# Kernel tuning notes

Hardware: AMD Instinct MI355X
Metric: run time of the kernel (lower is better)

## Reference

```python
import jax, jax.numpy as jnp
import numpy as np

# Scattering2D hyperparameters (kymatio-style Morlet filter bank)
J, L, M, N = 2, 8, 224, 224
SIGMA0 = 0.8
XI0 = 3.0 * np.pi / 4.0
SLANT = 4.0 / L


def _fold(h, k):
    """Fourier-domain subsampling / filter periodization: fold and average k x k blocks."""
    if k == 1:
        return h
    Mh, Nh = h.shape[-2], h.shape[-1]
    return h.reshape(h.shape[:-2] + (k, Mh // k, k, Nh // k)).mean(axis=(-4, -2))


def _freq_grid():
    wx = (2 * np.pi * np.fft.fftfreq(M)).astype(np.float64)[:, None]
    wy = (2 * np.pi * np.fft.fftfreq(N)).astype(np.float64)[None, :]
    return wx, wy


def _morlet_hat(theta, xi, sigma):
    wx, wy = _freq_grid()
    u = np.cos(theta) * wx + np.sin(theta) * wy
    v = -np.sin(theta) * wx + np.cos(theta) * wy
    gab = np.exp(-0.5 * sigma ** 2 * ((u - xi) ** 2 + (v / SLANT) ** 2))
    gauss = np.exp(-0.5 * sigma ** 2 * (u ** 2 + (v / SLANT) ** 2))
    kappa = np.exp(-0.5 * sigma ** 2 * xi ** 2)  # zero-mean Morlet correction
    return (gab - kappa * gauss).astype(np.float32)


def _build_filters():
    psi = {}
    for j in range(J):
        f = np.stack([_morlet_hat(l * np.pi / L, XI0 / 2 ** j, SIGMA0 * 2 ** j) for l in range(L)])
        psi[j] = [_fold(f, 2 ** r) for r in range(j + 1)]  # periodized to each resolution
    wx, wy = _freq_grid()
    sig_phi = SIGMA0 * 2 ** (J - 1)
    phi0 = np.exp(-0.5 * sig_phi ** 2 * (wx ** 2 + wy ** 2)).astype(np.float32)
    phi = [_fold(phi0, 2 ** r) for r in range(J)]
    return psi, phi


PSI, PHI = _build_filters()


def _scattering(x):
    # x: (B, C, M, N) float32 -> (B, C, K, M/2^J, N/2^J), K = 1 + J*L + L^2*J*(J-1)/2
    xh = jnp.fft.fft2(x)
    s0 = jnp.fft.ifft2(_fold(xh * PHI[0], 2 ** J)).real[..., None, :, :]
    s1s, s2s = [], []
    for j1 in range(J):
        # first order: bandpass, subsample to resolution j1, modulus
        u1h = _fold(xh[..., None, :, :] * PSI[j1][0], 2 ** j1)       # (B,C,L,M/2^j1,N/2^j1)
        u1 = jnp.abs(jnp.fft.ifft2(u1h))
        u1h2 = jnp.fft.fft2(u1)
        s1s.append(jnp.fft.ifft2(_fold(u1h2 * PHI[j1], 2 ** (J - j1))).real)
        for j2 in range(j1 + 1, J):
            # second order over all (theta1, theta2) pairs, vectorized over L x L
            u2h = _fold(u1h2[..., None, :, :] * PSI[j2][j1], 2 ** (j2 - j1))  # (B,C,L,L,.,.)
            u2 = jnp.abs(jnp.fft.ifft2(u2h))
            s2 = jnp.fft.ifft2(_fold(jnp.fft.fft2(u2) * PHI[j2], 2 ** (J - j2))).real
            s2s.append(s2.reshape(s2.shape[:2] + (L * L,) + s2.shape[-2:]))
    return jnp.concatenate([s0] + s1s + s2s, axis=2)


def setup_inputs() -> dict:
    key = jax.random.key(0)
    k1, k2, _ = jax.random.split(key, 3)
    x = jax.random.normal(k1, (16, 3, M, N), dtype=jnp.float32)
    W_last = jax.random.normal(k2, (1000, 243), dtype=jnp.float32) * 0.02
    b_last = jnp.zeros((1000,), dtype=jnp.float32)
    return {"x": x, "W_last": W_last, "b_last": b_last}


def reference(x, W_last, b_last):
    s = _scattering(x)                                   # (B, 3, 81, 56, 56)
    B = s.shape[0]
    s = s.reshape(B, s.shape[1] * s.shape[2], s.shape[3], s.shape[4])  # flatten(1,2)
    g = s.max(axis=(-2, -1))                             # global max pool -> (B, 243)
    return g @ W_last.T + b_last                         # (B, 1000)
```

## Files before the change

### kernel.cpp

```cpp
#include <hip/hip_runtime.h>
#include <math.h>

#define PI_D 3.14159265358979323846

#define IMG224 50176
#define IMG112 12544
static const size_t OFF_FT224F = 0;
static const size_t OFF_FT224I = 2048;
static const size_t OFF_FT112F = 4096;
static const size_t OFF_FT112I = 6144;
static const size_t OFF_FT56I  = 8192;
static const size_t OFF_PHW    = 8600;
static const size_t OFF_PSI   = 257152;
static const size_t OFF_PHI0  = 1059968;
static const size_t OFF_PHI1  = 1110144;
static const size_t OFF_GK    = 1122688;
static const size_t OFF_XH    = 1126784;
static const size_t OFF_POOL  = 5943680;

__device__ inline unsigned fkey(float v) {
    int b = __float_as_int(v);
    return (b >= 0) ? ((unsigned)b | 0x80000000u) : ~(unsigned)b;
}
__device__ inline float funkey(unsigned u) {
    int b = (u & 0x80000000u) ? (int)(u & 0x7fffffffu) : (int)~u;
    return __int_as_float(b);
}
__device__ inline void cmac(float2& a, float2 z, float2 w) {
    a.x += z.x * w.x - z.y * w.y;
    a.y += z.x * w.y + z.y * w.x;
}
__device__ inline float2 cmulc(float2 v, float c, float s) {
    return make_float2(v.x * c - v.y * s, v.x * s + v.y * c);
}

template<int SGN>
__device__ inline void fft16(float2* x) {
    const float C8  = 0.70710678118654752f;
    const float C16 = 0.92387953251128674f;
    const float S16 = 0.38268343236508977f;
    const float sg = (float)SGN;
    float2 g[16];
#pragma unroll
    for (int b = 0; b < 4; ++b) {
        float2 x0 = x[b], x1 = x[4 + b], x2 = x[8 + b], x3 = x[12 + b];
        float2 e0 = make_float2(x0.x + x2.x, x0.y + x2.y);
        float2 e1 = make_float2(x0.x - x2.x, x0.y - x2.y);
        float2 o0 = make_float2(x1.x + x3.x, x1.y + x3.y);
// ... 15 lines not shown
    g[14] = cmulc(g[14], -C8,  sg * C8);
    g[15] = cmulc(g[15], -C16, -sg * S16);
#pragma unroll
    for (int p = 0; p < 4; ++p) {
        float2 x0 = g[p], x1 = g[4 + p], x2 = g[8 + p], x3 = g[12 + p];
        float2 e0 = make_float2(x0.x + x2.x, x0.y + x2.y);
        float2 e1 = make_float2(x0.x - x2.x, x0.y - x2.y);
        float2 o0 = make_float2(x1.x + x3.x, x1.y + x3.y);
        float2 o1 = make_float2(x1.x - x3.x, x1.y - x3.y);
        float2 io1 = (SGN > 0) ? make_float2(-o1.y, o1.x) : make_float2(o1.y, -o1.x);
        x[p + 0]  = make_float2(e0.x + o0.x, e0.y + o0.y);
        x[p + 8]  = make_float2(e0.x - o0.x, e0.y - o0.y);
        x[p + 4]  = make_float2(e1.x + io1.x, e1.y + io1.y);
        x[p + 12] = make_float2(e1.x - io1.x, e1.y - io1.y);
    }
}

template<int SGN>
__device__ inline void fft8(float2* x) {
    const float C8 = 0.70710678118654752f;
    const float sg = (float)SGN;
    float2 E[4], O[4];
    {
        float2 e0 = make_float2(x[0].x + x[4].x, x[0].y + x[4].y);
        float2 e1 = make_float2(x[0].x - x[4].x, x[0].y - x[4].y);
        float2 o0 = make_float2(x[2].x + x[6].x, x[2].y + x[6].y);
        float2 o1 = make_float2(x[2].x - x[6].x, x[2].y - x[6].y);
        float2 io1 = (SGN > 0) ? make_float2(-o1.y, o1.x) : make_float2(o1.y, -o1.x);
        E[0] = make_float2(e0.x + o0.x, e0.y + o0.y);
        E[2] = make_float2(e0.x - o0.x, e0.y - o0.y);
        E[1] = make_float2(e1.x + io1.x, e1.y + io1.y);
        E[3] = make_float2(e1.x - io1.x, e1.y - io1.y);
    }
    {
        float2 e0 = make_float2(x[1].x + x[5].x, x[1].y + x[5].y);
        float2 e1 = make_float2(x[1].x - x[5].x, x[1].y - x[5].y);
        float2 o0 = make_float2(x[3].x + x[7].x, x[3].y + x[7].y);
        float2 o1 = make_float2(x[3].x - x[7].x, x[3].y - x[7].y);
        float2 io1 = (SGN > 0) ? make_float2(-o1.y, o1.x) : make_float2(o1.y, -o1.x);
        O[0] = make_float2(e0.x + o0.x, e0.y + o0.y);
        O[2] = make_float2(e0.x - o0.x, e0.y - o0.y);
        O[1] = make_float2(e1.x + io1.x, e1.y + io1.y);
        O[3] = make_float2(e1.x - io1.x, e1.y - io1.y);
    }
    float2 t0 = O[0];
    float2 t1 = cmulc(O[1], C8, sg * C8);
    float2 t2 = (SGN > 0) ? make_float2(-O[2].y, O[2].x) : make_float2(O[2].y, -O[2].x);
    float2 t3 = cmulc(O[3], -C8, sg * C8);
    x[0] = make_float2(E[0].x + t0.x, E[0].y + t0.y);
    x[4] = make_float2(E[0].x - t0.x, E[0].y - t0.y);
    x[1] = make_float2(E[1].x + t1.x, E[1].y + t1.y);
    x[5] = make_float2(E[1].x - t1.x, E[1].y - t1.y);
    x[2] = make_float2(E[2].x + t2.x, E[2].y + t2.y);
    x[6] = make_float2(E[2].x - t2.x, E[2].y - t2.y);
    x[3] = make_float2(E[3].x + t3.x, E[3].y + t3.y);
    x[7] = make_float2(E[3].x - t3.x, E[3].y - t3.y);
}

__global__ void k_fact(float2* o, int N1, int N2, double sign, double scale, int r2) {
    int base3 = N1 * N1 + N2 * N2 + N2 * N1;
    int total = base3 + (r2 ? 63 : 0);
    int N = N1 * N2;
    for (int i = blockIdx.x * blockDim.x + threadIdx.x; i < total; i += blockDim.x * gridDim.x) {
        double ang; double sc = 1.0;
        if (i < N1 * N1) {
            int n1 = i / N1, k1 = i % N1;
            ang = sign * 2.0 * PI_D * (double)((n1 * k1) % N1) / (double)N1;
        } else if (i < N1 * N1 + N2 * N2) {
            int j = i - N1 * N1; int n2 = j / N2, k2 = j % N2;
            ang = sign * 2.0 * PI_D * (double)((n2 * k2) % N2) / (double)N2;
            sc = scale;
// ... 24 lines not shown
    double wy = 2.0 * PI_D * fc / 224.0;
    double theta = (double)l * PI_D / 8.0;
    double xi = (3.0 * PI_D / 4.0) / (double)(1 << j);
    double sg = 0.8 * (double)(1 << j);
    double ct = cos(theta), st = sin(theta);
    double u = ct * wx + st * wy;
    double v = -st * wx + ct * wy;
    double vs = v / 0.5;
    double s2 = 0.5 * sg * sg;
    double gab = exp(-s2 * ((u - xi) * (u - xi) + vs * vs));
    double gau = exp(-s2 * (u * u + vs * vs));
    double kap = exp(-s2 * xi * xi);
    out[i] = (float)(gab - kap * gau);
}

__global__ void k_phi(float* phi0, float* phi1, float* taps) {
    int i = blockIdx.x * blockDim.x + threadIdx.x;
    const double sp = 1.6;
    const double s2 = 0.5 * sp * sp;
    if (i < IMG224) {
        int r = i / 224, c = i % 224;
        double fr = (r < 112) ? (double)r : (double)(r - 224);
        double fc = (c < 112) ? (double)c : (double)(c - 224);
        double wx = 2.0 * PI_D * fr / 224.0;
        double wy = 2.0 * PI_D * fc / 224.0;
        phi0[i] = (float)exp(-s2 * (wx * wx + wy * wy));
    } else if (i < IMG224 + IMG112) {
        int p = i - IMG224, a = p / 112, b = p % 112;
        double sum = 0.0;
        for (int ii = 0; ii < 2; ++ii)
            for (int jj = 0; jj < 2; ++jj) {
                int r = a + 112 * ii, c = b + 112 * jj;
                double fr = (r < 112) ? (double)r : (double)(r - 224);
                double fc = (c < 112) ? (double)c : (double)(c - 224);
                double wx = 2.0 * PI_D * fr / 224.0;
                double wy = 2.0 * PI_D * fc / 224.0;
                sum += exp(-s2 * (wx * wx + wy * wy));
            }
        phi1[p] = (float)(0.25 * sum);
    } else if (i < IMG224 + IMG112 + 16) {
        int m = i - (IMG224 + IMG112);
        double acc = 0.0;
        for (int k = 0; k < 112; ++k) {
            double fr0 = (double)k;
            double fr1 = (double)(k - 112);
            double w0 = 2.0 * PI_D * fr0 / 224.0;
            double w1 = 2.0 * PI_D * fr1 / 224.0;
            double F112 = 0.5 * (exp(-s2 * w0 * w0) + exp(-s2 * w1 * w1));
            acc += F112 * cos(2.0 * PI_D * (double)k * (double)m / 112.0);
        }
        taps[m] = (float)(acc / 112.0);
    }
}

__global__ void k_zero(unsigned* gk, int n) {
    int i = blockIdx.x * blockDim.x + threadIdx.x;
    if (i < n) gk[i] = 0u;
}

template<int N1, int N2, int TA, int FOLD, int BS, bool REAL, int SGN>
__global__ __launch_bounds__(BS) void rk(
    const void* __restrict__ inBase, int inShift,
    const float* __restrict__ fltBase, int fltMask,
    const float2* __restrict__ FT, float2* __restrict__ out,
    int swzImg, int inStride, int inOff)
{
// ... 46 lines not shown
                        float f = flt[idx];
                        re += v.x * f; im += v.y * f;
                    }
                Z[r * ZS + b] = make_float2(re * s, im * s);
            }
        }
    }
    __syncthreads();
    for (int idx = t; idx < TA * N2 * 2; idx += BS) {
        int r = idx / (N2 * 2);
        int rem = idx % (N2 * 2);
        int n2 = rem / 2, h = rem % 2;
        float2 xx[N1];
#pragma unroll
        for (int n1 = 0; n1 < N1; ++n1) xx[n1] = Z[r * ZS + n1 * N2 + n2];
        if constexpr (N1 == 16) fft16<SGN>(xx); else fft8<SGN>(xx);
#pragma unroll
        for (int kk = 0; kk < K1H; ++kk) {
            int k1 = h * K1H + kk;
            float2 tw = TW[n2 * N1 + k1];
            T[r * TS + n2 * (N1 + 1) + k1] = cmulc(xx[k1], tw.x, tw.y);
        }
    }
    __syncthreads();
    if constexpr (N2 == 14) {
        const float2* W7  = FT + N1 * N1 + N2 * N2 + N2 * N1;
        const float2* T14 = W7 + 49;
        for (int idx = t; idx < TA * N1; idx += BS) {
            int r = idx / N1, k1 = idx % N1;
            float2 E[7], O[7];
#pragma unroll
            for (int k = 0; k < 7; ++k) { E[k] = make_float2(0.f, 0.f); O[k] = make_float2(0.f, 0.f); }
            for (int m = 0; m < 7; ++m) {
                float2 te = T[r * TS + (2 * m) * (N1 + 1) + k1];
                float2 to = T[r * TS + (2 * m + 1) * (N1 + 1) + k1];
#pragma unroll
                for (int k = 0; k < 7; ++k) {
                    float2 w = W7[m * 7 + k];
                    cmac(E[k], te, w);
                    cmac(O[k], to, w);
                }
            }
#pragma unroll
            for (int k = 0; k < 14; ++k) {
                float2 tw = T14[k];
                float2 o_ = O[k % 7];
                float2 X = E[k % 7];
                X.x += o_.x * tw.x - o_.y * tw.y;
                X.y += o_.x * tw.y + o_.y * tw.x;
                Z[r * ZS + k1 + N1 * k] = X;
            }
        }
    } else {
        for (int idx = t; idx < TA * N1; idx += BS) {
            int r = idx / N1, k1 = idx % N1;
            float2 acc[N2];
#pragma unroll
            for (int kk = 0; kk < N2; ++kk) acc[kk] = make_float2(0.f, 0.f);
            for (int n2 = 0; n2 < N2; ++n2) {
                float2 tv = T[r * TS + n2 * (N1 + 1) + k1];
#pragma unroll
                for (int kk = 0; kk < N2; ++kk) cmac(acc[kk], tv, W2[n2 * N2 + kk]);
            }
#pragma unroll
            for (int kk = 0; kk < N2; ++kk) Z[r * ZS + k1 + N1 * kk] = acc[kk];
        }
    }
    __syncthreads();
#pragma unroll
    for (int r = 0; r < TA; ++r) {
        float2* o = out + ((size_t)gOut * N + (a0 + r)) * N;
        for (int b = t; b < N; b += BS) o[b] = Z[r * ZS + b];
    }
}

template<int N1, int N2, int SPLIT, int BS, int SGN>
__global__ __launch_bounds__(BS) void ck1(
    const float2* __restrict__ in, const float2* __restrict__ FT, float2* __restrict__ out)
{
    constexpr int N = N1 * N2;
// ... 18 lines not shown
        float2 tw = TW[n2 * N1 + k1];
        float2 r0 = cmulc(a0[k1], tw.x, tw.y);
        float2 r1 = cmulc(a1[k1], tw.x, tw.y);
        *reinterpret_cast<float4*>(&out[((size_t)g * N + (k1 * N2 + n2)) * N + b0]) =
            make_float4(r0.x, r0.y, r1.x, r1.y);
    }
}

template<int N1, int N2, int SPLIT, int MODE, int BS>
__global__ __launch_bounds__(BS) void ck2(
    const float2* __restrict__ in, const float2* __restrict__ FT,
    float2* __restrict__ outc, float* __restrict__ outr)
{
    constexpr int N = N1 * N2;
    constexpr int NC = N / SPLIT;
    const float2* W2 = FT + N1 * N1;
    const int g = blockIdx.x / SPLIT, half = blockIdx.x % SPLIT;
    const int k1 = blockIdx.y, t = threadIdx.x;
    if (2 * t >= NC) return;
    const int b0 = 2 * t + half * NC;
    const float2* I = in + (size_t)g * N * N;
    if constexpr (N2 == 14) {
        const float2* W7  = FT + N1 * N1 + N2 * N2 + N2 * N1;
        const float2* T14 = W7 + 49;
        float2 E0[7], E1[7], O0[7], O1[7];
#pragma unroll
        for (int k = 0; k < 7; ++k) {
            E0[k] = make_float2(0.f, 0.f); E1[k] = make_float2(0.f, 0.f);
            O0[k] = make_float2(0.f, 0.f); O1[k] = make_float2(0.f, 0.f);
        }
#pragma unroll
        for (int m = 0; m < 7; ++m) {
            float4 ve = *reinterpret_cast<const float4*>(&I[(size_t)(k1 * 14 + 2 * m) * N + b0]);
            float4 vo = *reinterpret_cast<const float4*>(&I[(size_t)(k1 * 14 + 2 * m + 1) * N + b0]);
            float2 ve0 = make_float2(ve.x, ve.y), ve1 = make_float2(ve.z, ve.w);
            float2 vo0 = make_float2(vo.x, vo.y), vo1 = make_float2(vo.z, vo.w);
#pragma unroll
            for (int k = 0; k < 7; ++k) {
                float2 w = W7[m * 7 + k];
                cmac(E0[k], ve0, w); cmac(E1[k], ve1, w);
                cmac(O0[k], vo0, w); cmac(O1[k], vo1, w);
            }
        }
#pragma unroll
        for (int k = 0; k < 14; ++k) {
            float2 tw = T14[k];
            float2 r0 = E0[k % 7], r1 = E1[k % 7];
            float2 o0 = O0[k % 7], o1 = O1[k % 7];
            r0.x += o0.x * tw.x - o0.y * tw.y;
            r0.y += o0.x * tw.y + o0.y * tw.x;
            r1.x += o1.x * tw.x - o1.y * tw.y;
            r1.y += o1.x * tw.y + o1.y * tw.x;
            if (MODE == 0) {
                *reinterpret_cast<float4*>(&outc[((size_t)g * N + (k1 + N1 * k)) * N + b0]) =
                    make_float4(r0.x, r0.y, r1.x, r1.y);
            } else {
                size_t o = ((size_t)g * N + (k1 + N1 * k)) * N + b0;
                outr[o]     = sqrtf(r0.x * r0.x + r0.y * r0.y);
                outr[o + 1] = sqrtf(r1.x * r1.x + r1.y * r1.y);
            }
        }
    } else {
        float2 acc[N2][2];
#pragma unroll
        for (int k2 = 0; k2 < N2; ++k2) { acc[k2][0] = make_float2(0.f, 0.f); acc[k2][1] = make_float2(0.f, 0.f); }
#pragma unroll
        for (int n2 = 0; n2 < N2; ++n2) {
            float4 v = *reinterpret_cast<const float4*>(&I[(size_t)(k1 * N2 + n2) * N + b0]);
            float2 v0 = make_float2(v.x, v.y), v1 = make_float2(v.z, v.w);
#pragma unroll
            for (int k2 = 0; k2 < N2; ++k2) {
                float2 w = W2[n2 * N2 + k2];
                cmac(acc[k2][0], v0, w);
                cmac(acc[k2][1], v1, w);
            }
        }
        if (MODE == 0) {
#pragma unroll
            for (int k2 = 0; k2 < N2; ++k2)
                *reinterpret_cast<float4*>(&outc[((size_t)g * N + (k1 + N1 * k2)) * N + b0]) =
                    make_float4(acc[k2][0].x, acc[k2][0].y, acc[k2][1].x, acc[k2][1].y);
        } else {
#pragma unroll
            for (int k2 = 0; k2 < N2; ++k2) {
                size_t o = ((size_t)g * N + (k1 + N1 * k2)) * N + b0;
                outr[o]     = sqrtf(acc[k2][0].x * acc[k2][0].x + acc[k2][0].y * acc[k2][0].y);
                outr[o + 1] = sqrtf(acc[k2][1].x * acc[k2][1].x + acc[k2][1].y * acc[k2][1].y);
            }
        }
    }
}

template<int SGN, int BS, int EPI>
__device__ inline void fft112_2d(float2* Z, const float2* __restrict__ FT, int t)
{
    constexpr int ZS = 113;
    constexpr int NCH = (112 * 16 + BS - 1) / BS;
    const float2* W2 = FT + 256;
    const float2* TW = FT + 256 + 49;
    const float s7 = W2[0].x;
    float wr[3][3], wi[3][3];
#pragma unroll
    for (int m = 1; m <= 3; ++m)
#pragma unroll
        for (int k = 1; k <= 3; ++k) {
            float2 w = W2[m * 7 + k];
            wr[m - 1][k - 1] = w.x;
            wi[m - 1][k - 1] = w.y;
        }
    for (int idx = t; idx < 112 * 7; idx += BS) {
        int r = idx % 112, n2 = idx / 112;
        float2 xx[16];
#pragma unroll
        for (int n1 = 0; n1 < 16; ++n1) xx[n1] = Z[r * ZS + n1 * 7 + n2];
        fft16<SGN>(xx);
#pragma unroll
        for (int k1 = 0; k1 < 16; ++k1) {
            float2 tw = TW[n2 * 16 + k1];
            Z[r * ZS + k1 * 7 + n2] = cmulc(xx[k1], tw.x, tw.y);
        }
    }
    __syncthreads();
    {
        float2 tv[NCH][7];
#pragma unroll
        for (int c = 0; c < NCH; ++c) {
            int idx = c * BS + t;
            if (idx < 112 * 16) {
                int r = idx >> 4, k1 = idx & 15;
#pragma unroll
                for (int m = 0; m < 7; ++m) tv[c][m] = Z[r * ZS + k1 * 7 + m];
            }
        }
        __syncthreads();
#pragma unroll
        for (int c = 0; c < NCH; ++c) {
            int idx = c * BS + t;
            if (idx < 112 * 16) {
                int r = idx >> 4, k1 = idx & 15;
                float2 t0 = tv[c][0];
                float2 a1 = make_float2(tv[c][1].x + tv[c][6].x, tv[c][1].y + tv[c][6].y);
                float2 b1 = make_float2(tv[c][1].x - tv[c][6].x, tv[c][1].y - tv[c][6].y);
                float2 a2 = make_float2(tv[c][2].x + tv[c][5].x, tv[c][2].y + tv[c][5].y);
                float2 b2 = make_float2(tv[c][2].x - tv[c][5].x, tv[c][2].y - tv[c][5].y);
                float2 a3 = make_float2(tv[c][3].x + tv[c][4].x, tv[c][3].y + tv[c][4].y);
                float2 b3 = make_float2(tv[c][3].x - tv[c][4].x, tv[c][3].y - tv[c][4].y);
                float bx = s7 * t0.x, by = s7 * t0.y;
                Z[r * ZS + k1] = make_float2(s7 * (t0.x + a1.x + a2.x + a3.x),
                                             s7 * (t0.y + a1.y + a2.y + a3.y));
#pragma unroll
                for (int k = 0; k < 3; ++k) {
                    float Px = wr[0][k] * a1.x + wr[1][k] * a2.x + wr[2][k] * a3.x;
                    float Py = wr[0][k] * a1.y + wr[1][k] * a2.y + wr[2][k] * a3.y;
                    float Qx = wi[0][k] * b1.x + wi[1][k] * b2.x + wi[2][k] * b3.x;
                    float Qy = wi[0][k] * b1.y + wi[1][k] * b2.y + wi[2][k] * b3.y;
                    Z[r * ZS + k1 + 16 * (k + 1)] = make_float2(bx + Px - Qy, by + Py + Qx);
                    Z[r * ZS + k1 + 16 * (6 - k)] = make_float2(bx + Px + Qy, by + Py - Qx);
                }
            }
        }
    }
    __syncthreads();
    for (int idx = t; idx < 112 * 7; idx += BS) {
        int b = idx % 112, n2 = idx / 112;
        float2 xx[16];
#pragma unroll
        for (int n1 = 0; n1 < 16; ++n1) xx[n1] = Z[(n1 * 7 + n2) * ZS + b];
        fft16<SGN>(xx);
#pragma unroll
        for (int k1 = 0; k1 < 16; ++k1) {
            float2 tw = TW[n2 * 16 + k1];
            Z[(k1 * 7 + n2) * ZS + b] = cmulc(xx[k1], tw.x, tw.y);
        }
// ... 4 lines not shown
#pragma unroll
        for (int c = 0; c < NCH; ++c) {
            int idx = c * BS + t;
            if (idx < 112 * 16) {
                int b = idx >> 4, k1 = idx & 15;
#pragma unroll
                for (int m = 0; m < 7; ++m) tv[c][m] = Z[(k1 * 7 + m) * ZS + b];
            }
        }
        __syncthreads();
#pragma unroll
        for (int c = 0; c < NCH; ++c) {
            int idx = c * BS + t;
            if (idx < 112 * 16) {
                int b = idx >> 4, k1 = idx & 15;
                float2 t0 = tv[c][0];
                float2 a1 = make_float2(tv[c][1].x + tv[c][6].x, tv[c][1].y + tv[c][6].y);
                float2 b1 = make_float2(tv[c][1].x - tv[c][6].x, tv[c][1].y - tv[c][6].y);
                float2 a2 = make_float2(tv[c][2].x + tv[c][5].x, tv[c][2].y + tv[c][5].y);
                float2 b2 = make_float2(tv[c][2].x - tv[c][5].x, tv[c][2].y - tv[c][5].y);
                float2 a3 = make_float2(tv[c][3].x + tv[c][4].x, tv[c][3].y + tv[c][4].y);
                float2 b3 = make_float2(tv[c][3].x - tv[c][4].x, tv[c][3].y - tv[c][4].y);
                float bxr = s7 * t0.x, byr = s7 * t0.y;
                {
                    float X = s7 * (t0.x + a1.x + a2.x + a3.x);
                    float Y = s7 * (t0.y + a1.y + a2.y + a3.y);
                    Z[k1 * ZS + b] = EPI ? make_float2(sqrtf(X * X + Y * Y), 0.f)
                                         : make_float2(X, Y);
                }
#pragma unroll
                for (int k = 0; k < 3; ++k) {
                    float Px = wr[0][k] * a1.x + wr[1][k] * a2.x + wr[2][k] * a3.x;
                    float Py = wr[0][k] * a1.y + wr[1][k] * a2.y + wr[2][k] * a3.y;
                    float Qx = wi[0][k] * b1.x + wi[1][k] * b2.x + wi[2][k] * b3.x;
                    float Qy = wi[0][k] * b1.y + wi[1][k] * b2.y + wi[2][k] * b3.y;
                    float X1 = bxr + Px - Qy, Y1 = byr + Py + Qx;
                    float X2 = bxr + Px + Qy, Y2 = byr + Py - Qx;
                    Z[(k1 + 16 * (k + 1)) * ZS + b] =
                        EPI ? make_float2(sqrtf(X1 * X1 + Y1 * Y1), 0.f) : make_float2(X1, Y1);
                    Z[(k1 + 16 * (6 - k)) * ZS + b] =
                        EPI ? make_float2(sqrtf(X2 * X2 + Y2 * Y2), 0.f) : make_float2(X2, Y2);
                }
            }
        }
    }
    __syncthreads();
}

template<int BS>
__global__ __launch_bounds__(BS) void sc2pipe(
    const float2* __restrict__ inBase, const float* __restrict__ psiBase,
    const float* __restrict__ taps, const float2* __restrict__ FTI,
    unsigned* __restrict__ gk, int slotBase, int inStride, int subShift)
{
    constexpr int ZS = 113;
    __shared__ float2 Z[112 * ZS];
// ... 53 lines not shown
            int rb = r0 + m; rb -= (rb >= 112) ? 112 : 0;
            acc += gw[m] * (Ft[ra * 57 + j] + Ft[rb * 57 + j]);
        }
        mx = fmaxf(mx, acc);
    }
    for (int off = 32; off > 0; off >>= 1) mx = fmaxf(mx, __shfl_down(mx, off, 64));
    if ((t & 63) == 0) red[t >> 6] = mx;
    __syncthreads();
    if (t == 0) {
#pragma unroll
        for (int w = 1; w < BS / 64; ++w) mx = fmaxf(mx, red[w]);
        atomicMax(&gk[img * 81 + slotBase + sub], fkey(mx));
    }
}

template<int FOLD, int BS>
__global__ __launch_bounds__(BS) void s56max(
    const float2* __restrict__ in, const float* __restrict__ flt,
    const float2* __restrict__ FT, unsigned* __restrict__ gk,
    int slotBase, int slotShift, int slotMask)
{
    constexpr int N = 56, NIN = 56 * FOLD, ZS = 57;
    __shared__ float2 Z[N * ZS];
    __shared__ float2 T[N * ZS];
    __shared__ float red[BS / 64];
    const float2* W2 = FT + 64;
    const float2* TW = FT + 64 + 49;
    const int g = blockIdx.x, t = threadIdx.x;
    const float2* I = in + (size_t)g * NIN * NIN;
    const float s = 1.0f / (float)(FOLD * FOLD);
#pragma unroll 4
    for (int idx = t; idx < N * N; idx += BS) {
        int r = idx / N, b = idx % N;
        float re = 0.f, im = 0.f;
#pragma unroll
        for (int i = 0; i < FOLD; ++i)
#pragma unroll
            for (int j = 0; j < FOLD; ++j) {
                int p = (r + N * i) * NIN + (b + N * j);
                float2 v = I[p];
                float f = flt[p];
                re += v.x * f; im += v.y * f;
            }
        Z[r * ZS + b] = make_float2(re * s, im * s);
    }
    __syncthreads();
    for (int idx = t; idx < 7 * N; idx += BS) {
        int n2 = idx / N, r = idx % N;
        float2 xx[8];
#pragma unroll
        for (int n1 = 0; n1 < 8; ++n1) xx[n1] = Z[r * ZS + n1 * 7 + n2];
        fft8<1>(xx);
#pragma unroll
        for (int k1 = 0; k1 < 8; ++k1) {
            float2 tw = TW[n2 * 8 + k1];
            T[r * ZS + k1 * 7 + n2] = cmulc(xx[k1], tw.x, tw.y);
        }
    }
    __syncthreads();
    for (int idx = t; idx < 8 * N; idx += BS) {
        int k1 = idx / N, r = idx % N;
        float2 tv[7];
#pragma unroll
        for (int n2 = 0; n2 < 7; ++n2) tv[n2] = T[r * ZS + k1 * 7 + n2];
#pragma unroll
        for (int k2 = 0; k2 < 7; ++k2) {
            float2 acc = make_float2(0.f, 0.f);
#pragma unroll
            for (int n2 = 0; n2 < 7; ++n2) cmac(acc, tv[n2], W2[n2 * 7 + k2]);
            Z[r * ZS + k1 + 8 * k2] = acc;
        }
    }
    __syncthreads();
    for (int idx = t; idx < 7 * N; idx += BS) {
        int n2 = idx / N, b = idx % N;
        float2 xx[8];
#pragma unroll
        for (int n1 = 0; n1 < 8; ++n1) xx[n1] = Z[(n1 * 7 + n2) * ZS + b];
        fft8<1>(xx);
#pragma unroll
        for (int k1 = 0; k1 < 8; ++k1) {
            float2 tw = TW[n2 * 8 + k1];
            T[(k1 * 7 + n2) * ZS + b] = cmulc(xx[k1], tw.x, tw.y);
        }
    }
    __syncthreads();
    float m = -INFINITY;
    for (int idx = t; idx < 8 * N; idx += BS) {
        int k1 = idx / N, b = idx % N;
        float2 tv[7];
#pragma unroll
        for (int n2 = 0; n2 < 7; ++n2) tv[n2] = T[(k1 * 7 + n2) * ZS + b];
#pragma unroll
        for (int k2 = 0; k2 < 7; ++k2) {
            float re = 0.f;
#pragma unroll
            for (int n2 = 0; n2 < 7; ++n2) {
                float2 w = W2[n2 * 7 + k2];
                re += tv[n2].x * w.x - tv[n2].y * w.y;
            }
            m = fmaxf(m, re);
        }
    }
    for (int off = 32; off > 0; off >>= 1) m = fmaxf(m, __shfl_down(m, off, 64));
    if ((t & 63) == 0) red[t >> 6] = m;
    __syncthreads();
    if (t == 0) {
#pragma unroll
        for (int w = 1; w < BS / 64; ++w) m = fmaxf(m, red[w]);
        int slot = slotBase + ((g >> slotShift) * 81) + (g & slotMask);
        atomicMax(&gk[slot], fkey(m));
    }
}

__global__ void k_linear(const unsigned* __restrict__ gk, const float* __restrict__ Wl,
                         const float* __restrict__ bl, float* __restrict__ out)
{
    int i = blockIdx.x * blockDim.x + threadIdx.x;
    if (i >= 16 * 1000) return;
    int b = i / 1000, o = i % 1000;
    float s = bl[o];
    for (int f = 0; f < 243; ++f)
        s += funkey(gk[b * 243 + f]) * Wl[o * 243 + f];
    out[i] = s;
}

extern "C" void kernel_launch(void* const* d_in, const int* in_sizes, int n_in,
                              void* d_out, int out_size, void* d_ws, size_t ws_size,
                              hipStream_t stream)
{
    const float* x  = (const float*)d_in[0];
    const float* Wl = (const float*)d_in[1];
    const float* bl = (const float*)d_in[2];
    float* out = (float*)d_out;
    float* ws = (float*)d_ws;

    float2* FT224F = (float2*)(ws + OFF_FT224F);
    float2* FT224I = (float2*)(ws + OFF_FT224I);
    float2* FT112F = (float2*)(ws + OFF_FT112F);
    float2* FT112I = (float2*)(ws + OFF_FT112I);
    float2* FT56I  = (float2*)(ws + OFF_FT56I);
    float* TAPS = ws + OFF_PHW;
    float* PSI0 = ws + OFF_PSI;
    float* PSI1 = ws + OFF_PSI + 8 * IMG224;
    float* PHI0 = ws + OFF_PHI0;
    float* PHI1 = ws + OFF_PHI1;
    unsigned* GK = (unsigned*)(ws + OFF_GK);
    float2* XH  = (float2*)(ws + OFF_XH);
    float* A0  = ws + OFF_POOL;
    float* A1  = A0 + 9633792;
    float* A23 = A1 + 9633792;

    k_fact<<<4, 256, 0, stream>>>(FT224F, 16, 14, -1.0, 1.0, 1);
    k_fact<<<4, 256, 0, stream>>>(FT224I, 16, 14,  1.0, 1.0 / 224.0, 1);
    k_fact<<<4, 256, 0, stream>>>(FT112F, 16, 7,  -1.0, 1.0, 0);
    k_fact<<<4, 256, 0, stream>>>(FT112I, 16, 7,   1.0, 1.0 / 112.0, 0);
    k_fact<<<1, 256, 0, stream>>>(FT56I,  8, 7,    1.0, 1.0 / 56.0, 0);
    k_psi<<<(16 * IMG224 + 255) / 256, 256, 0, stream>>>(ws + OFF_PSI);
    k_phi<<<(IMG224 + IMG112 + 16 + 255) / 256, 256, 0, stream>>>(PHI0, PHI1, TAPS);
    k_zero<<<(3888 + 255) / 256, 256, 0, stream>>>(GK, 3888);

    rk<16, 14, 4, 1, 128, true, -1><<<dim3(48, 56), 128, 0, stream>>>(x, 0, nullptr, 0, FT224F, (float2*)A0, 0, 0, 0);
    ck1<16, 14, 2, 64, -1><<<dim3(96, 14), 64, 0, stream>>>((float2*)A0, FT224F, (float2*)A1);
    ck2<16, 14, 2, 0, 64><<<dim3(96, 16), 64, 0, stream>>>((float2*)A1, FT224F, XH, nullptr);

    s56max<4, 256><<<48, 256, 0, stream>>>(XH, PHI0, FT56I, GK, 0, 0, 0);

    sc2pipe<1024><<<384, 1024, 0, stream>>>(XH, PSI1, TAPS, FT112I, GK, 9, 1, 3);

    for (int c = 0; c < 4; ++c) {
        rk<16, 14, 4, 1, 128, false, 1><<<dim3(96, 56), 128, 0, stream>>>(
            XH, 1, PSI0 + (size_t)(2 * c) * IMG224, 1, FT224I, (float2*)A0, -1, 0, 0);
        ck1<16, 14, 2, 64, 1><<<dim3(192, 14), 64, 0, stream>>>((float2*)A0, FT224I, (float2*)A1);
        ck2<16, 14, 2, 1, 64><<<dim3(192, 16), 64, 0, stream>>>((float2*)A1, FT224I, nullptr, A23);
        rk<16, 14, 4, 1, 128, true, -1><<<dim3(96, 56), 128, 0, stream>>>(A23, 0, nullptr, 0, FT224F, (float2*)A0, 0, 0, 0);
        ck1<16, 14, 2, 64, -1><<<dim3(192, 14), 64, 0, stream>>>((float2*)A0, FT224F, (float2*)A1);
        ck2<16, 14, 2, 0, 64><<<dim3(192, 16), 64, 0, stream>>>((float2*)A1, FT224F, (float2*)A0, nullptr);
        s56max<4, 256><<<96, 256, 0, stream>>>((float2*)A0, PHI0, FT56I, GK, 1 + 2 * c, 1, 1);
        sc2pipe<1024><<<768, 1024, 0, stream>>>((float2*)A0, PSI1, TAPS, FT112I, GK, 17 + 16 * c, 2, 4);
    }

    k_linear<<<(16000 + 255) / 256, 256, 0, stream>>>(GK, Wl, bl, out);
}
```

Measured before the change: 1.068 ms.

## Replace Fourier-domain lowpass/fold/iFFT with spatial separable conv and use symmetric DFT7

The order-0 and order-1 lowpass outputs are now computed directly in the spatial domain as a separable 23-tap circular convolution, evaluated only at every fourth row and column, with precomputed taps. This replaces the Fourier multiply, fold and 56x56 inverse FFT (s56max). The order-1 pass runs on the real modulus image before its forward FFT. The column-pass DFT7 in ck2 now uses the shared symmetric-pair dft7 helper instead of a dense 7x7 complex matmul. The unused phi filters and 112/56 twiddle tables are dropped. The spatial conv truncates the Gaussian kernel to 11 taps per side, which introduces a small approximation.

```diff
diff --git a/kernel.cpp b/kernel.cpp
--- a/kernel.cpp
+++ b/kernel.cpp
@@ -9,11 +9,8 @@
 static const size_t OFF_FT224I = 2048;
 static const size_t OFF_FT112F = 4096;
 static const size_t OFF_FT112I = 6144;
-static const size_t OFF_FT56I  = 8192;
 static const size_t OFF_PHW    = 8600;
 static const size_t OFF_PSI   = 257152;
-static const size_t OFF_PHI0  = 1059968;
-static const size_t OFF_PHI1  = 1110144;
 static const size_t OFF_GK    = 1122688;
 static const size_t OFF_XH    = 1126784;
 static const size_t OFF_POOL  = 5943680;
@@ -32,6 +29,39 @@
 }
 __device__ inline float2 cmulc(float2 v, float c, float s) {
     return make_float2(v.x * c - v.y * s, v.x * s + v.y * c);
+}
+
+struct C7 { float s; float wr[3][3]; float wi[3][3]; };
+__device__ inline void ld7(const float2* __restrict__ W7, C7& c) {
+    c.s = W7[0].x;
+#pragma unroll
+    for (int m = 1; m <= 3; ++m)
+#pragma unroll
+        for (int k = 1; k <= 3; ++k) {
+            float2 w = W7[m * 7 + k];
+            c.wr[m - 1][k - 1] = w.x;
+            c.wi[m - 1][k - 1] = w.y;
+        }
+}
+__device__ inline void dft7(const C7& c, const float2 t[7], float2 X[7]) {
+    float2 a1 = make_float2(t[1].x + t[6].x, t[1].y + t[6].y);
+    float2 b1 = make_float2(t[1].x - t[6].x, t[1].y - t[6].y);
+    float2 a2 = make_float2(t[2].x + t[5].x, t[2].y + t[5].y);
+    float2 b2 = make_float2(t[2].x - t[5].x, t[2].y - t[5].y);
+    float2 a3 = make_float2(t[3].x + t[4].x, t[3].y + t[4].y);
+    float2 b3 = make_float2(t[3].x - t[4].x, t[3].y - t[4].y);
+    float bx = c.s * t[0].x, by = c.s * t[0].y;
+    X[0] = make_float2(c.s * (t[0].x + a1.x + a2.x + a3.x),
+                       c.s * (t[0].y + a1.y + a2.y + a3.y));
+#pragma unroll
+    for (int k = 0; k < 3; ++k) {
+        float Px = c.wr[0][k] * a1.x + c.wr[1][k] * a2.x + c.wr[2][k] * a3.x;
+        float Py = c.wr[0][k] * a1.y + c.wr[1][k] * a2.y + c.wr[2][k] * a3.y;
+        float Qx = c.wi[0][k] * b1.x + c.wi[1][k] * b2.x + c.wi[2][k] * b3.x;
+        float Qy = c.wi[0][k] * b1.y + c.wi[1][k] * b2.y + c.wi[2][k] * b3.y;
+        X[k + 1] = make_float2(bx + Px - Qy, by + Py + Qx);
+        X[6 - k] = make_float2(bx + Px + Qy, by + Py - Qx);
+    }
 }
 
 template<int SGN>
@@ -77,47 +107,6 @@
         x[p + 4]  = make_float2(e1.x + io1.x, e1.y + io1.y);
         x[p + 12] = make_float2(e1.x - io1.x, e1.y - io1.y);
     }
-}
-
-template<int SGN>
-__device__ inline void fft8(float2* x) {
-    const float C8 = 0.70710678118654752f;
-    const float sg = (float)SGN;
-    float2 E[4], O[4];
-    {
-        float2 e0 = make_float2(x[0].x + x[4].x, x[0].y + x[4].y);
-        float2 e1 = make_float2(x[0].x - x[4].x, x[0].y - x[4].y);
-        float2 o0 = make_float2(x[2].x + x[6].x, x[2].y + x[6].y);
-        float2 o1 = make_float2(x[2].x - x[6].x, x[2].y - x[6].y);
-        float2 io1 = (SGN > 0) ? make_float2(-o1.y, o1.x) : make_float2(o1.y, -o1.x);
-        E[0] = make_float2(e0.x + o0.x, e0.y + o0.y);
-        E[2] = make_float2(e0.x - o0.x, e0.y - o0.y);
-        E[1] = make_float2(e1.x + io1.x, e1.y + io1.y);
-        E[3] = make_float2(e1.x - io1.x, e1.y - io1.y);
-    }
-    {
-        float2 e0 = make_float2(x[1].x + x[5].x, x[1].y + x[5].y);
-        float2 e1 = make_float2(x[1].x - x[5].x, x[1].y - x[5].y);
-        float2 o0 = make_float2(x[3].x + x[7].x, x[3].y + x[7].y);
-        float2 o1 = make_float2(x[3].x - x[7].x, x[3].y - x[7].y);
-        float2 io1 = (SGN > 0) ? make_float2(-o1.y, o1.x) : make_float2(o1.y, -o1.x);
-        O[0] = make_float2(e0.x + o0.x, e0.y + o0.y);
-        O[2] = make_float2(e0.x - o0.x, e0.y - o0.y);
-        O[1] = make_float2(e1.x + io1.x, e1.y + io1.y);
-        O[3] = make_float2(e1.x - io1.x, e1.y - io1.y);
-    }
-    float2 t0 = O[0];
-    float2 t1 = cmulc(O[1], C8, sg * C8);
-    float2 t2 = (SGN > 0) ? make_float2(-O[2].y, O[2].x) : make_float2(O[2].y, -O[2].x);
-    float2 t3 = cmulc(O[3], -C8, sg * C8);
-    x[0] = make_float2(E[0].x + t0.x, E[0].y + t0.y);
-    x[4] = make_float2(E[0].x - t0.x, E[0].y - t0.y);
-    x[1] = make_float2(E[1].x + t1.x, E[1].y + t1.y);
-    x[5] = make_float2(E[1].x - t1.x, E[1].y - t1.y);
-    x[2] = make_float2(E[2].x + t2.x, E[2].y + t2.y);
-    x[6] = make_float2(E[2].x - t2.x, E[2].y - t2.y);
-    x[3] = make_float2(E[3].x + t3.x, E[3].y + t3.y);
-    x[7] = make_float2(E[3].x - t3.x, E[3].y - t3.y);
 }
 
 __global__ void k_fact(float2* o, int N1, int N2, double sign, double scale, int r2) {
@@ -172,42 +161,27 @@
     out[i] = (float)(gab - kap * gau);
 }
 
-__global__ void k_phi(float* phi0, float* phi1, float* taps) {
+__global__ void k_taps(float* taps) {
     int i = blockIdx.x * blockDim.x + threadIdx.x;
-    const double sp = 1.6;
-    const double s2 = 0.5 * sp * sp;
-    if (i < IMG224) {
-        int r = i / 224, c = i % 224;
-        double fr = (r < 112) ? (double)r : (double)(r - 224);
-        double fc = (c < 112) ? (double)c : (double)(c - 224);
-        double wx = 2.0 * PI_D * fr / 224.0;
-        double wy = 2.0 * PI_D * fc / 224.0;
-        phi0[i] = (float)exp(-s2 * (wx * wx + wy * wy));
-    } else if (i < IMG224 + IMG112) {
-        int p = i - IMG224, a = p / 112, b = p % 112;
-        double sum = 0.0;
-        for (int ii = 0; ii < 2; ++ii)
-            for (int jj = 0; jj < 2; ++jj) {
-                int r = a + 112 * ii, c = b + 112 * jj;
-                double fr = (r < 112) ? (double)r : (double)(r - 224);
-                double fc = (c < 112) ? (double)c : (double)(c - 224);
-                double wx = 2.0 * PI_D * fr / 224.0;
-                double wy = 2.0 * PI_D * fc / 224.0;
-                sum += exp(-s2 * (wx * wx + wy * wy));
-            }
-        phi1[p] = (float)(0.25 * sum);
-    } else if (i < IMG224 + IMG112 + 16) {
-        int m = i - (IMG224 + IMG112);
+    const double s2 = 0.5 * 1.6 * 1.6;
+    if (i < 16) {
         double acc = 0.0;
         for (int k = 0; k < 112; ++k) {
-            double fr0 = (double)k;
-            double fr1 = (double)(k - 112);
-            double w0 = 2.0 * PI_D * fr0 / 224.0;
-            double w1 = 2.0 * PI_D * fr1 / 224.0;
-            double F112 = 0.5 * (exp(-s2 * w0 * w0) + exp(-s2 * w1 * w1));
-            acc += F112 * cos(2.0 * PI_D * (double)k * (double)m / 112.0);
-        }
-        taps[m] = (float)(acc / 112.0);
+            double w0 = 2.0 * PI_D * (double)k / 224.0;
+            double w1 = 2.0 * PI_D * (double)(k - 112) / 224.0;
+            double F = 0.5 * (exp(-s2 * w0 * w0) + exp(-s2 * w1 * w1));
+            acc += F * cos(2.0 * PI_D * (double)k * (double)i / 112.0);
+        }
+        taps[i] = (float)(acc / 112.0);
+    } else if (i < 32) {
+        int m = i - 16;
+        double acc = 0.0;
+        for (int k = 0; k < 224; ++k) {
+            double fr = (k < 112) ? (double)k : (double)(k - 224);
+            double w = 2.0 * PI_D * fr / 224.0;
+            acc += exp(-s2 * w * w) * cos(2.0 * PI_D * (double)k * (double)m / 224.0);
+        }
+        taps[i] = (float)(acc / 224.0);
     }
 }
 
@@ -284,7 +258,7 @@
         float2 xx[N1];
 #pragma unroll
         for (int n1 = 0; n1 < N1; ++n1) xx[n1] = Z[r * ZS + n1 * N2 + n2];
-        if constexpr (N1 == 16) fft16<SGN>(xx); else fft8<SGN>(xx);
+        fft16<SGN>(xx);
 #pragma unroll
         for (int kk = 0; kk < K1H; ++kk) {
             int k1 = h * K1H + kk;
@@ -293,7 +267,7 @@
         }
     }
     __syncthreads();
-    if constexpr (N2 == 14) {
+    {
         const float2* W7  = FT + N1 * N1 + N2 * N2 + N2 * N1;
         const float2* T14 = W7 + 49;
         for (int idx = t; idx < TA * N1; idx += BS) {
@@ -320,20 +294,6 @@
                 X.y += o_.x * tw.y + o_.y * tw.x;
                 Z[r * ZS + k1 + N1 * k] = X;
             }
-        }
-    } else {
-        for (int idx = t; idx < TA * N1; idx += BS) {
-            int r = idx / N1, k1 = idx % N1;
-            float2 acc[N2];
-#pragma unroll
-            for (int kk = 0; kk < N2; ++kk) acc[kk] = make_float2(0.f, 0.f);
-            for (int n2 = 0; n2 < N2; ++n2) {
-                float2 tv = T[r * TS + n2 * (N1 + 1) + k1];
-#pragma unroll
-                for (int kk = 0; kk < N2; ++kk) cmac(acc[kk], tv, W2[n2 * N2 + kk]);
-            }
-#pragma unroll
-            for (int kk = 0; kk < N2; ++kk) Z[r * ZS + k1 + N1 * kk] = acc[kk];
         }
     }
     __syncthreads();
@@ -382,79 +342,48 @@
 {
     constexpr int N = N1 * N2;
     constexpr int NC = N / SPLIT;
-    const float2* W2 = FT + N1 * N1;
     const int g = blockIdx.x / SPLIT, half = blockIdx.x % SPLIT;
     const int k1 = blockIdx.y, t = threadIdx.x;
     if (2 * t >= NC) return;
     const int b0 = 2 * t + half * NC;
     const float2* I = in + (size_t)g * N * N;
-    if constexpr (N2 == 14) {
-        const float2* W7  = FT + N1 * N1 + N2 * N2 + N2 * N1;
-        const float2* T14 = W7 + 49;
-        float2 E0[7], E1[7], O0[7], O1[7];
-#pragma unroll
-        for (int k = 0; k < 7; ++k) {
-            E0[k] = make_float2(0.f, 0.f); E1[k] = make_float2(0.f, 0.f);
-            O0[k] = make_float2(0.f, 0.f); O1[k] = make_float2(0.f, 0.f);
-        }
-#pragma unroll
-        for (int m = 0; m < 7; ++m) {
-            float4 ve = *reinterpret_cast<const float4*>(&I[(size_t)(k1 * 14 + 2 * m) * N + b0]);
-            float4 vo = *reinterpret_cast<const float4*>(&I[(size_t)(k1 * 14 + 2 * m + 1) * N + b0]);
-            float2 ve0 = make_float2(ve.x, ve.y), ve1 = make_float2(ve.z, ve.w);
-            float2 vo0 = make_float2(vo.x, vo.y), vo1 = make_float2(vo.z, vo.w);
-#pragma unroll
-            for (int k = 0; k < 7; ++k) {
-                float2 w = W7[m * 7 + k];
-                cmac(E0[k], ve0, w); cmac(E1[k], ve1, w);
-                cmac(O0[k], vo0, w); cmac(O1[k], vo1, w);
-            }
-        }
-#pragma unroll
-        for (int k = 0; k < 14; ++k) {
-            float2 tw = T14[k];
-            float2 r0 = E0[k % 7], r1 = E1[k % 7];
-            float2 o0 = O0[k % 7], o1 = O1[k % 7];
-            r0.x += o0.x * tw.x - o0.y * tw.y;
-            r0.y += o0.x * tw.y + o0.y * tw.x;
-            r1.x += o1.x * tw.x - o1.y * tw.y;
-            r1.y += o1.x * tw.y + o1.y * tw.x;
-            if (MODE == 0) {
-                *reinterpret_cast<float4*>(&outc[((size_t)g * N + (k1 + N1 * k)) * N + b0]) =
-                    make_float4(r0.x, r0.y, r1.x, r1.y);
-            } else {
-                size_t o = ((size_t)g * N + (k1 + N1 * k)) * N + b0;
-                outr[o]     = sqrtf(r0.x * r0.x + r0.y * r0.y);
-                outr[o + 1] = sqrtf(r1.x * r1.x + r1.y * r1.y);
-            }
-        }
-    } else {
-        float2 acc[N2][2];
-#pragma unroll
-        for (int k2 = 0; k2 < N2; ++k2) { acc[k2][0] = make_float2(0.f, 0.f); acc[k2][1] = make_float2(0.f, 0.f); }
-#pragma unroll
-        for (int n2 = 0; n2 < N2; ++n2) {
-            float4 v = *reinterpret_cast<const float4*>(&I[(size_t)(k1 * N2 + n2) * N + b0]);
-            float2 v0 = make_float2(v.x, v.y), v1 = make_float2(v.z, v.w);
-#pragma unroll
-            for (int k2 = 0; k2 < N2; ++k2) {
-                float2 w = W2[n2 * N2 + k2];
-                cmac(acc[k2][0], v0, w);
-                cmac(acc[k2][1], v1, w);
-            }
-        }
+    const float2* W7  = FT + N1 * N1 + N2 * N2 + N2 * N1;
+    const float2* T14 = W7 + 49;
+    C7 c7; ld7(W7, c7);
+    float2 te0[7], te1[7], E0[7], E1[7];
+#pragma unroll
+    for (int m = 0; m < 7; ++m) {
+        float4 ve = *reinterpret_cast<const float4*>(&I[(size_t)(k1 * 14 + 2 * m) * N + b0]);
+        te0[m] = make_float2(ve.x, ve.y);
+        te1[m] = make_float2(ve.z, ve.w);
+    }
+    dft7(c7, te0, E0);
+    dft7(c7, te1, E1);
+    float2 to0[7], to1[7], O0[7], O1[7];
+#pragma unroll
+    for (int m = 0; m < 7; ++m) {
+        float4 vo = *reinterpret_cast<const float4*>(&I[(size_t)(k1 * 14 + 2 * m + 1) * N + b0]);
+        to0[m] = make_float2(vo.x, vo.y);
+        to1[m] = make_float2(vo.z, vo.w);
+    }
+    dft7(c7, to0, O0);
+    dft7(c7, to1, O1);
+#pragma unroll
+    for (int k = 0; k < 14; ++k) {
+        float2 tw = T14[k];
+        float2 r0 = E0[k % 7], r1 = E1[k % 7];
+        float2 o0 = O0[k % 7], o1 = O1[k % 7];
+        r0.x += o0.x * tw.x - o0.y * tw.y;
+        r0.y += o0.x * tw.y + o0.y * tw.x;
+        r1.x += o1.x * tw.x - o1.y * tw.y;
+        r1.y += o1.x * tw.y + o1.y * tw.x;
         if (MODE == 0) {
-#pragma unroll
-            for (int k2 = 0; k2 < N2; ++k2)
-                *reinterpret_cast<float4*>(&outc[((size_t)g * N + (k1 + N1 * k2)) * N + b0]) =
-                    make_float4(acc[k2][0].x, acc[k2][0].y, acc[k2][1].x, acc[k2][1].y);
+            *reinterpret_cast<float4*>(&outc[((size_t)g * N + (k1 + N1 * k)) * N + b0]) =
+                make_float4(r0.x, r0.y, r1.x, r1.y);
         } else {
-#pragma unroll
-            for (int k2 = 0; k2 < N2; ++k2) {
-                size_t o = ((size_t)g * N + (k1 + N1 * k2)) * N + b0;
-                outr[o]     = sqrtf(acc[k2][0].x * acc[k2][0].x + acc[k2][0].y * acc[k2][0].y);
-                outr[o + 1] = sqrtf(acc[k2][1].x * acc[k2][1].x + acc[k2][1].y * acc[k2][1].y);
-            }
+            size_t o = ((size_t)g * N + (k1 + N1 * k)) * N + b0;
+            outr[o]     = sqrtf(r0.x * r0.x + r0.y * r0.y);
+            outr[o + 1] = sqrtf(r1.x * r1.x + r1.y * r1.y);
         }
     }
 }
@@ -466,16 +395,7 @@
     constexpr int NCH = (112 * 16 + BS - 1) / BS;
     const float2* W2 = FT + 256;
     const float2* TW = FT + 256 + 49;
-    const float s7 = W2[0].x;
-    float wr[3][3], wi[3][3];
-#pragma unroll
-    for (int m = 1; m <= 3; ++m)
-#pragma unroll
-        for (int k = 1; k <= 3; ++k) {
-            float2 w = W2[m * 7 + k];
-            wr[m - 1][k - 1] = w.x;
-            wi[m - 1][k - 1] = w.y;
-        }
+    C7 c7; ld7(W2, c7);
     for (int idx = t; idx < 112 * 7; idx += BS) {
         int r = idx % 112, n2 = idx / 112;
         float2 xx[16];
@@ -506,25 +426,10 @@
             int idx = c * BS + t;
             if (idx < 112 * 16) {
                 int r = idx >> 4, k1 = idx & 15;
-                float2 t0 = tv[c][0];
-                float2 a1 = make_float2(tv[c][1].x + tv[c][6].x, tv[c][1].y + tv[c][6].y);
-                float2 b1 = make_float2(tv[c][1].x - tv[c][6].x, tv[c][1].y - tv[c][6].y);
-                float2 a2 = make_float2(tv[c][2].x + tv[c][5].x, tv[c][2].y + tv[c][5].y);
-                float2 b2 = make_float2(tv[c][2].x - tv[c][5].x, tv[c][2].y - tv[c][5].y);
-                float2 a3 = make_float2(tv[c][3].x + tv[c][4].x, tv[c][3].y + tv[c][4].y);
-                float2 b3 = make_float2(tv[c][3].x - tv[c][4].x, tv[c][3].y - tv[c][4].y);
-                float bx = s7 * t0.x, by = s7 * t0.y;
-                Z[r * ZS + k1] = make_float2(s7 * (t0.x + a1.x + a2.x + a3.x),
-                                             s7 * (t0.y + a1.y + a2.y + a3.y));
-#pragma unroll
-                for (int k = 0; k < 3; ++k) {
-                    float Px = wr[0][k] * a1.x + wr[1][k] * a2.x + wr[2][k] * a3.x;
-                    float Py = wr[0][k] * a1.y + wr[1][k] * a2.y + wr[2][k] * a3.y;
-                    float Qx = wi[0][k] * b1.x + wi[1][k] * b2.x + wi[2][k] * b3.x;
-                    float Qy = wi[0][k] * b1.y + wi[1][k] * b2.y + wi[2][k] * b3.y;
-                    Z[r * ZS + k1 + 16 * (k + 1)] = make_float2(bx + Px - Qy, by + Py + Qx);
-                    Z[r * ZS + k1 + 16 * (6 - k)] = make_float2(bx + Px + Qy, by + Py - Qx);
-                }
+                float2 X[7];
+                dft7(c7, tv[c], X);
+#pragma unroll
+                for (int k = 0; k < 7; ++k) Z[r * ZS + k1 + 16 * k] = X[k];
             }
         }
     }
@@ -559,32 +464,13 @@
             int idx = c * BS + t;
             if (idx < 112 * 16) {
                 int b = idx >> 4, k1 = idx & 15;
-                float2 t0 = tv[c][0];
-                float2 a1 = make_float2(tv[c][1].x + tv[c][6].x, tv[c][1].y + tv[c][6].y);
-                float2 b1 = make_float2(tv[c][1].x - tv[c][6].x, tv[c][1].y - tv[c][6].y);
-                float2 a2 = make_float2(tv[c][2].x + tv[c][5].x, tv[c][2].y + tv[c][5].y);
-                float2 b2 = make_float2(tv[c][2].x - tv[c][5].x, tv[c][2].y - tv[c][5].y);
-                float2 a3 = make_float2(tv[c][3].x + tv[c][4].x, tv[c][3].y + tv[c][4].y);
-                float2 b3 = make_float2(tv[c][3].x - tv[c][4].x, tv[c][3].y - tv[c][4].y);
-                float bxr = s7 * t0.x, byr = s7 * t0.y;
-                {
-                    float X = s7 * (t0.x + a1.x + a2.x + a3.x);
-                    float Y = s7 * (t0.y + a1.y + a2.y + a3.y);
-                    Z[k1 * ZS + b] = EPI ? make_float2(sqrtf(X * X + Y * Y), 0.f)
-                                         : make_float2(X, Y);
-                }
-#pragma unroll
-                for (int k = 0; k < 3; ++k) {
-                    float Px = wr[0][k] * a1.x + wr[1][k] * a2.x + wr[2][k] * a3.x;
-                    float Py = wr[0][k] * a1.y + wr[1][k] * a2.y + wr[2][k] * a3.y;
-                    float Qx = wi[0][k] * b1.x + wi[1][k] * b2.x + wi[2][k] * b3.x;
-                    float Qy = wi[0][k] * b1.y + wi[1][k] * b2.y + wi[2][k] * b3.y;
-                    float X1 = bxr + Px - Qy, Y1 = byr + Py + Qx;
-                    float X2 = bxr + Px + Qy, Y2 = byr + Py - Qx;
-                    Z[(k1 + 16 * (k + 1)) * ZS + b] =
-                        EPI ? make_float2(sqrtf(X1 * X1 + Y1 * Y1), 0.f) : make_float2(X1, Y1);
-                    Z[(k1 + 16 * (6 - k)) * ZS + b] =
-                        EPI ? make_float2(sqrtf(X2 * X2 + Y2 * Y2), 0.f) : make_float2(X2, Y2);
+                float2 X[7];
+                dft7(c7, tv[c], X);
+#pragma unroll
+                for (int k = 0; k < 7; ++k) {
+                    Z[(k1 + 16 * k) * ZS + b] =
+                        EPI ? make_float2(sqrtf(X[k].x * X[k].x + X[k].y * X[k].y), 0.f)
+                            : X[k];
                 }
             }
         }
@@ -668,102 +554,53 @@
     }
 }
 
-template<int FOLD, int BS>
-__global__ __launch_bounds__(BS) void s56max(
-    const float2* __restrict__ in, const float* __restrict__ flt,
-    const float2* __restrict__ FT, unsigned* __restrict__ gk,
-    int slotBase, int slotShift, int slotMask)
-{
-    constexpr int N = 56, NIN = 56 * FOLD, ZS = 57;
-    __shared__ float2 Z[N * ZS];
-    __shared__ float2 T[N * ZS];
+template<int BS>
+__global__ __launch_bounds__(BS) void s1conv(
+    const float* __restrict__ inBase, const float* __restrict__ taps,
+    unsigned* __restrict__ gk, int slotBase, int slotShift, int slotMask)
+{
+    __shared__ float R[224 * 56];
     __shared__ float red[BS / 64];
-    const float2* W2 = FT + 64;
-    const float2* TW = FT + 64 + 49;
     const int g = blockIdx.x, t = threadIdx.x;
-    const float2* I = in + (size_t)g * NIN * NIN;
-    const float s = 1.0f / (float)(FOLD * FOLD);
-#pragma unroll 4
-    for (int idx = t; idx < N * N; idx += BS) {
-        int r = idx / N, b = idx % N;
-        float re = 0.f, im = 0.f;
-#pragma unroll
-        for (int i = 0; i < FOLD; ++i)
-#pragma unroll
-            for (int j = 0; j < FOLD; ++j) {
-                int p = (r + N * i) * NIN + (b + N * j);
-                float2 v = I[p];
-                float f = flt[p];
-                re += v.x * f; im += v.y * f;
-            }
-        Z[r * ZS + b] = make_float2(re * s, im * s);
-    }
-    __syncthreads();
-    for (int idx = t; idx < 7 * N; idx += BS) {
-        int n2 = idx / N, r = idx % N;
-        float2 xx[8];
-#pragma unroll
-        for (int n1 = 0; n1 < 8; ++n1) xx[n1] = Z[r * ZS + n1 * 7 + n2];
-        fft8<1>(xx);
-#pragma unroll
-        for (int k1 = 0; k1 < 8; ++k1) {
-            float2 tw = TW[n2 * 8 + k1];
-            T[r * ZS + k1 * 7 + n2] = cmulc(xx[k1], tw.x, tw.y);
-        }
-    }
-    __syncthreads();
-    for (int idx = t; idx < 8 * N; idx += BS) {
-        int k1 = idx / N, r = idx % N;
-        float2 tv[7];
-#pragma unroll
-        for (int n2 = 0; n2 < 7; ++n2) tv[n2] = T[r * ZS + k1 * 7 + n2];
-#pragma unroll
-        for (int k2 = 0; k2 < 7; ++k2) {
-            float2 acc = make_float2(0.f, 0.f);
-#pragma unroll
-            for (int n2 = 0; n2 < 7; ++n2) cmac(acc, tv[n2], W2[n2 * 7 + k2]);
-            Z[r * ZS + k1 + 8 * k2] = acc;
-        }
-    }
-    __syncthreads();
-    for (int idx = t; idx < 7 * N; idx += BS) {
-        int n2 = idx / N, b = idx % N;
-        float2 xx[8];
-#pragma unroll
-        for (int n1 = 0; n1 < 8; ++n1) xx[n1] = Z[(n1 * 7 + n2) * ZS + b];
-        fft8<1>(xx);
-#pragma unroll
-        for (int k1 = 0; k1 < 8; ++k1) {
-            float2 tw = TW[n2 * 8 + k1];
-            T[(k1 * 7 + n2) * ZS + b] = cmulc(xx[k1], tw.x, tw.y);
-        }
-    }
-    __syncthreads();
-    float m = -INFINITY;
-    for (int idx = t; idx < 8 * N; idx += BS) {
-        int k1 = idx / N, b = idx % N;
-        float2 tv[7];
-#pragma unroll
-        for (int n2 = 0; n2 < 7; ++n2) tv[n2] = T[(k1 * 7 + n2) * ZS + b];
-#pragma unroll
-        for (int k2 = 0; k2 < 7; ++k2) {
-            float re = 0.f;
-#pragma unroll
-            for (int n2 = 0; n2 < 7; ++n2) {
-                float2 w = W2[n2 * 7 + k2];
-                re += tv[n2].x * w.x - tv[n2].y * w.y;
-            }
-            m = fmaxf(m, re);
-        }
-    }
-    for (int off = 32; off > 0; off >>= 1) m = fmaxf(m, __shfl_down(m, off, 64));
-    if ((t & 63) == 0) red[t >> 6] = m;
+    const float* u = inBase + (size_t)g * 50176;
+    float gw[12];
+#pragma unroll
+    for (int i = 0; i < 12; ++i) gw[i] = taps[i];
+    for (int idx = t; idx < 224 * 56; idx += BS) {
+        int j = idx % 56, r = idx / 56;
+        int c0 = 4 * j;
+        const float* row = u + r * 224;
+        float acc = gw[0] * row[c0];
+#pragma unroll
+        for (int m = 1; m <= 11; ++m) {
+            int cm = c0 - m; cm += (cm < 0) ? 224 : 0;
+            int cq = c0 + m; cq -= (cq >= 224) ? 224 : 0;
+            acc += gw[m] * (row[cm] + row[cq]);
+        }
+        R[r * 56 + j] = acc;
+    }
+    __syncthreads();
+    float mx = -INFINITY;
+    for (int idx = t; idx < 56 * 56; idx += BS) {
+        int j = idx % 56, ip = idx / 56;
+        int r0 = 4 * ip;
+        float acc = gw[0] * R[r0 * 56 + j];
+#pragma unroll
+        for (int m = 1; m <= 11; ++m) {
+            int ra = r0 - m; ra += (ra < 0) ? 224 : 0;
+            int rb = r0 + m; rb -= (rb >= 224) ? 224 : 0;
+            acc += gw[m] * (R[ra * 56 + j] + R[rb * 56 + j]);
+        }
+        mx = fmaxf(mx, acc);
+    }
+    for (int off = 32; off > 0; off >>= 1) mx = fmaxf(mx, __shfl_down(mx, off, 64));
+    if ((t & 63) == 0) red[t >> 6] = mx;
     __syncthreads();
     if (t == 0) {
 #pragma unroll
-        for (int w = 1; w < BS / 64; ++w) m = fmaxf(m, red[w]);
+        for (int w = 1; w < BS / 64; ++w) mx = fmaxf(mx, red[w]);
         int slot = slotBase + ((g >> slotShift) * 81) + (g & slotMask);
-        atomicMax(&gk[slot], fkey(m));
+        atomicMax(&gk[slot], fkey(mx));
     }
 }
 
@@ -791,14 +628,10 @@
 
     float2* FT224F = (float2*)(ws + OFF_FT224F);
     float2* FT224I = (float2*)(ws + OFF_FT224I);
-    float2* FT112F = (float2*)(ws + OFF_FT112F);
     float2* FT112I = (float2*)(ws + OFF_FT112I);
-    float2* FT56I  = (float2*)(ws + OFF_FT56I);
     float* TAPS = ws + OFF_PHW;
     float* PSI0 = ws + OFF_PSI;
     float* PSI1 = ws + OFF_PSI + 8 * IMG224;
-    float* PHI0 = ws + OFF_PHI0;
-    float* PHI1 = ws + OFF_PHI1;
     unsigned* GK = (unsigned*)(ws + OFF_GK);
     float2* XH  = (float2*)(ws + OFF_XH);
     float* A0  = ws + OFF_POOL;
@@ -807,18 +640,16 @@
 
     k_fact<<<4, 256, 0, stream>>>(FT224F, 16, 14, -1.0, 1.0, 1);
     k_fact<<<4, 256, 0, stream>>>(FT224I, 16, 14,  1.0, 1.0 / 224.0, 1);
-    k_fact<<<4, 256, 0, stream>>>(FT112F, 16, 7,  -1.0, 1.0, 0);
     k_fact<<<4, 256, 0, stream>>>(FT112I, 16, 7,   1.0, 1.0 / 112.0, 0);
-    k_fact<<<1, 256, 0, stream>>>(FT56I,  8, 7,    1.0, 1.0 / 56.0, 0);
     k_psi<<<(16 * IMG224 + 255) / 256, 256, 0, stream>>>(ws + OFF_PSI);
-    k_phi<<<(IMG224 + IMG112 + 16 + 255) / 256, 256, 0, stream>>>(PHI0, PHI1, TAPS);
+    k_taps<<<1, 64, 0, stream>>>(TAPS);
     k_zero<<<(3888 + 255) / 256, 256, 0, stream>>>(GK, 3888);
 
     rk<16, 14, 4, 1, 128, true, -1><<<dim3(48, 56), 128, 0, stream>>>(x, 0, nullptr, 0, FT224F, (float2*)A0, 0, 0, 0);
     ck1<16, 14, 2, 64, -1><<<dim3(96, 14), 64, 0, stream>>>((float2*)A0, FT224F, (float2*)A1);
     ck2<16, 14, 2, 0, 64><<<dim3(96, 16), 64, 0, stream>>>((float2*)A1, FT224F, XH, nullptr);
 
-    s56max<4, 256><<<48, 256, 0, stream>>>(XH, PHI0, FT56I, GK, 0, 0, 0);
+    s1conv<256><<<48, 256, 0, stream>>>(x, TAPS + 16, GK, 0, 0, 0);
 
     sc2pipe<1024><<<384, 1024, 0, stream>>>(XH, PSI1, TAPS, FT112I, GK, 9, 1, 3);
 
@@ -827,10 +658,10 @@
             XH, 1, PSI0 + (size_t)(2 * c) * IMG224, 1, FT224I, (float2*)A0, -1, 0, 0);
         ck1<16, 14, 2, 64, 1><<<dim3(192, 14), 64, 0, stream>>>((float2*)A0, FT224I, (float2*)A1);
         ck2<16, 14, 2, 1, 64><<<dim3(192, 16), 64, 0, stream>>>((float2*)A1, FT224I, nullptr, A23);
+        s1conv<256><<<96, 256, 0, stream>>>(A23, TAPS + 16, GK, 1 + 2 * c, 1, 1);
         rk<16, 14, 4, 1, 128, true, -1><<<dim3(96, 56), 128, 0, stream>>>(A23, 0, nullptr, 0, FT224F, (float2*)A0, 0, 0, 0);
         ck1<16, 14, 2, 64, -1><<<dim3(192, 14), 64, 0, stream>>>((float2*)A0, FT224F, (float2*)A1);
         ck2<16, 14, 2, 0, 64><<<dim3(192, 16), 64, 0, stream>>>((float2*)A1, FT224F, (float2*)A0, nullptr);
-        s56max<4, 256><<<96, 256, 0, stream>>>((float2*)A0, PHI0, FT56I, GK, 1 + 2 * c, 1, 1);
         sc2pipe<1024><<<768, 1024, 0, stream>>>((float2*)A0, PSI1, TAPS, FT112I, GK, 17 + 16 * c, 2, 4);
     }
 
```

New measurement: 1.297 ms. 1.21x slower.
